# Kernel optimization log

Hardware: AMD Instinct MI355X
Metric: run time of the kernel (lower is better)

The kernel has to match this reference:

```python
import jax, jax.numpy as jnp
import numpy as np

N = 100000      # nodes
E = 1600000     # edges
G = 128         # graphs in batch
F_IN = 128
HID = 32
NCLS = 10


def _gcn_conv(x, src, dst, norm, W, b):
    # x: [N, Fin] -> [N, Fout]; src/dst/norm include self-loops: [E+N]
    h = x @ W                                   # dense transform first (Fout=32 < Fin)
    msg = h[src] * norm[:, None]                # gather + edge normalization
    out = jax.ops.segment_sum(msg, dst, num_segments=N)  # scatter-add
    return out + b


def setup_inputs() -> dict:
    key = jax.random.key(0)
    ks = jax.random.split(key, 10)
    x = jax.random.normal(ks[0], (N, F_IN), dtype=jnp.float32)
    edge_index = jax.random.randint(ks[1], (2, E), 0, N, dtype=jnp.int64)
    batch = jnp.sort(jax.random.randint(ks[2], (N,), 0, G, dtype=jnp.int64))
    s = 1.0 / np.sqrt(F_IN)
    W0 = jax.random.normal(ks[3], (F_IN, HID), dtype=jnp.float32) * s
    b0 = jnp.zeros((HID,), dtype=jnp.float32)
    sh = 1.0 / np.sqrt(HID)
    W1 = jax.random.normal(ks[4], (HID, HID), dtype=jnp.float32) * sh
    b1 = jnp.zeros((HID,), dtype=jnp.float32)
    W2 = jax.random.normal(ks[5], (HID, HID), dtype=jnp.float32) * sh
    b2 = jnp.zeros((HID,), dtype=jnp.float32)
    Wl = jax.random.normal(ks[6], (HID, NCLS), dtype=jnp.float32) * sh
    bl = jnp.zeros((NCLS,), dtype=jnp.float32)
    return {"x": x, "edge_index": edge_index, "batch": batch,
            "W0": W0, "b0": b0, "W1": W1, "b1": b1,
            "W2": W2, "b2": b2, "Wl": Wl, "bl": bl}


def reference(x, edge_index, batch, W0, b0, W1, b1, W2, b2, Wl, bl):
    # Self-loop augmented edge list (PyG GCNConv default: add_self_loops=True)
    loop = jnp.arange(N, dtype=edge_index.dtype)
    src = jnp.concatenate([edge_index[0], loop])    # [E+N]
    dst = jnp.concatenate([edge_index[1], loop])
    # Symmetric normalization D^{-1/2} (A+I) D^{-1/2}
    deg = jax.ops.segment_sum(jnp.ones_like(src, dtype=x.dtype), dst, num_segments=N)
    dinv = jax.lax.rsqrt(deg)                       # deg >= 1 thanks to self-loops
    norm = dinv[src] * dinv[dst]                    # [E+N]

    h = x
    for (W, b) in ((W0, b0), (W1, b1), (W2, b2)):
        h = jax.nn.relu(_gcn_conv(h, src, dst, norm, W, b))

    # global mean pool over graphs
    sums = jax.ops.segment_sum(h, batch, num_segments=G)           # [G, HID]
    cnts = jax.ops.segment_sum(jnp.ones((N,), h.dtype), batch, num_segments=G)
    pooled = sums / jnp.maximum(cnts, 1.0)[:, None]

    logits = jax.nn.relu(pooled @ Wl + bl)
    return jax.nn.log_softmax(logits, axis=1)
```

## Files before the change

### kernel.cpp

```cpp
#include <hip/hip_runtime.h>
#include <hip/hip_bf16.h>

#define NN 100000
#define NE 1600000
#define NG 128
#define FIN 128
#define HID 32
#define NCLS 10

#define EG4 (NE / 4)

#define NSL 32
#define GPS (EG4 / NSL)
#define RS 8
#define SUBN (NN / RS)
#define CSRGRID (RS * NSL)
#define CSR_T 1024

#define PAD 16
#define NEP (NE + NN * PAD + 64)

#define SCAN_B 1024
#define NB ((NN + SCAN_B - 1) / SCAN_B)

#define POOL_CHUNK 512
#define POOL_SEG 16
#define POOL_GSPAN 32
#define POOL_GRID ((NN + POOL_CHUNK - 1) / POOL_CHUNK)

#define G0_NODES 64
#define G0_GRID ((NN + G0_NODES - 1) / G0_NODES)
#define XPAD 136

#define AGG_GRID (NN / 4)
#define AGF_GRID (NN / 16)

typedef int int4v __attribute__((ext_vector_type(4)));
typedef __attribute__((ext_vector_type(8))) short short8;
typedef __attribute__((ext_vector_type(4))) float f32x4;

__device__ inline unsigned short f2bf(float f) {
    unsigned int u = __float_as_uint(f);
    unsigned int r = u + 0x7FFFu + ((u >> 16) & 1u);
    return (unsigned short)(r >> 16);
}
__device__ inline float bf2f(unsigned short v) {
    return __uint_as_float(((unsigned int)v) << 16);
}

__global__ void k_init(float* __restrict__ gsum, float* __restrict__ gcnt,
                       unsigned short* __restrict__ tzero,
                       unsigned short* __restrict__ hzero) {
    int i = blockIdx.x * blockDim.x + threadIdx.x;
    if (i < NG * HID) gsum[i] = 0.f;
    if (i < NG) gcnt[i] = 0.f;
    if (i < HID) { tzero[i] = 0; hzero[i] = 0; }
}

__global__ __launch_bounds__(CSR_T) void k_hist3(const int* __restrict__ dst,
                                                 unsigned char* __restrict__ partial) {
    const int r = blockIdx.x & (RS - 1);
    const int s = blockIdx.x >> 3;
    const int node0 = r * SUBN;
    __shared__ int lcnt[SUBN];
    for (int k = threadIdx.x; k < SUBN; k += CSR_T) lcnt[k] = 0;
    __syncthreads();
    const int g1 = (s + 1) * GPS;
    for (int g = s * GPS + threadIdx.x; g < g1; g += CSR_T) {
        const int4v d = *((const int4v*)dst + g);
        unsigned k;
        k = (unsigned)(d.x - node0); if (k < SUBN) atomicAdd(&lcnt[k], 1);
        k = (unsigned)(d.y - node0); if (k < SUBN) atomicAdd(&lcnt[k], 1);
        k = (unsigned)(d.z - node0); if (k < SUBN) atomicAdd(&lcnt[k], 1);
        k = (unsigned)(d.w - node0); if (k < SUBN) atomicAdd(&lcnt[k], 1);
    }
    __syncthreads();
    for (int k = threadIdx.x; k < SUBN; k += CSR_T)
        partial[s * NN + node0 + k] = (unsigned char)lcnt[k];
}

__global__ void k_scanA(unsigned char* __restrict__ partial, int* __restrict__ row_ptr,
                        int* __restrict__ bsum, float* __restrict__ dinv,
                        int* __restrict__ deg) {
    __shared__ int lds[SCAN_B];
    int i = blockIdx.x * SCAN_B + threadIdx.x;
    int pv = 0;
    if (i < NN) {
        int run = 0;
#pragma unroll
        for (int s = 0; s < NSL; s++) {
            int c = partial[s * NN + i];
            partial[s * NN + i] = (unsigned char)run;
            run += c;
        }
        deg[i] = run;
        dinv[i] = rsqrtf((float)run + 1.0f);
        pv = (run + PAD - 1) & ~(PAD - 1);
    }
    lds[threadIdx.x] = pv;
    __syncthreads();
    int val = pv;
    for (int off = 1; off < SCAN_B; off <<= 1) {
        int u = 0;
        if ((int)threadIdx.x >= off) u = lds[threadIdx.x - off];
        __syncthreads();
        if ((int)threadIdx.x >= off) { val += u; lds[threadIdx.x] = val; }
        __syncthreads();
    }
    if (i < NN) row_ptr[i] = val - pv;
    if (threadIdx.x == SCAN_B - 1) bsum[blockIdx.x] = val;
}

__global__ void k_scanB(int* __restrict__ bsum) {
    __shared__ int lds[128];
    int t = threadIdx.x;
    int v = (t < NB) ? bsum[t] : 0;
    lds[t] = v;
    __syncthreads();
    int val = v;
    for (int off = 1; off < 128; off <<= 1) {
        int u = 0;
        if (t >= off) u = lds[t - off];
        __syncthreads();
        if (t >= off) { val += u; lds[t] = val; }
        __syncthreads();
    }
    if (t < NB) bsum[t] = val - v;
}

__global__ void k_scanC(int* __restrict__ row_ptr, const int* __restrict__ bsum,
                        const int* __restrict__ deg, int* __restrict__ csr_src) {
    int i = blockIdx.x * SCAN_B + threadIdx.x;
    if (i < NN) {
        int r = row_ptr[i] + bsum[blockIdx.x];
        row_ptr[i] = r;
        int d = deg[i];
        int pd = (d + PAD - 1) & ~(PAD - 1);
        if (i == NN - 1) row_ptr[NN] = r + pd;
        for (int j = r + d; j < r + pd; j++) csr_src[j] = NN;
    }
}

__global__ __launch_bounds__(CSR_T) void k_scat3(const int* __restrict__ src,
                                                 const int* __restrict__ dst,
                                                 const int* __restrict__ row_ptr,
                                                 const unsigned char* __restrict__ pref,
                                                 int* __restrict__ csr_src) {
    const int r = blockIdx.x & (RS - 1);
    const int s = blockIdx.x >> 3;
    const int node0 = r * SUBN;
    __shared__ int lcur[SUBN];
    for (int k = threadIdx.x; k < SUBN; k += CSR_T)
        lcur[k] = row_ptr[node0 + k] + (int)pref[s * NN + node0 + k];
    __syncthreads();
    const int g1 = (s + 1) * GPS;
    for (int g = s * GPS + threadIdx.x; g < g1; g += CSR_T) {
        const int4v d = *((const int4v*)dst + g);
        const int4v sx = *((const int4v*)src + g);
        unsigned k;
        k = (unsigned)(d.x - node0); if (k < SUBN) { int p = atomicAdd(&lcur[k], 1); csr_src[p] = sx.x; }
        k = (unsigned)(d.y - node0); if (k < SUBN) { int p = atomicAdd(&lcur[k], 1); csr_src[p] = sx.y; }
        k = (unsigned)(d.z - node0); if (k < SUBN) { int p = atomicAdd(&lcur[k], 1); csr_src[p] = sx.z; }
        k = (unsigned)(d.w - node0); if (k < SUBN) { int p = atomicAdd(&lcur[k], 1); csr_src[p] = sx.w; }
    }
}

__global__ void k_gemm0(const float* __restrict__ x, const float* __restrict__ W,
                        const float* __restrict__ dinv, unsigned short* __restrict__ t) {
    __shared__ __align__(16) unsigned short x_lds[G0_NODES][XPAD];
    __shared__ __align__(16) unsigned short wt_lds[HID][XPAD];
    const int tid = threadIdx.x;
    const int node0 = blockIdx.x * G0_NODES;

#pragma unroll
    for (int r = 0; r < 8; r++) {
        int q = tid + 256 * r;
        int row = q >> 5;
        int c4 = q & 31;
        float4 xv = {0.f, 0.f, 0.f, 0.f};
        int node = node0 + row;
        if (node < NN) xv = ((const float4*)(x + (size_t)node * FIN))[c4];
        ushort4 b;
        b.x = f2bf(xv.x); b.y = f2bf(xv.y); b.z = f2bf(xv.z); b.w = f2bf(xv.w);
        *(ushort4*)&x_lds[row][c4 * 4] = b;
    }
#pragma unroll
    for (int r = 0; r < 16; r++) {
        int q = tid + 256 * r;
        int k = q >> 5, n = q & 31;
        wt_lds[n][k] = f2bf(W[q]);
    }
    __syncthreads();

    const int w = tid >> 6;
    const int lane = tid & 63;
    const int row = lane & 15;
    const int kg = lane >> 4;
    const int w16 = w * 16;

    f32x4 acc0 = {0.f, 0.f, 0.f, 0.f};
    f32x4 acc1 = {0.f, 0.f, 0.f, 0.f};
#pragma unroll
    for (int s = 0; s < 4; s++) {
        short8 a  = *(const short8*)&x_lds[w16 + row][s * 32 + kg * 8];
        short8 b0 = *(const short8*)&wt_lds[row][s * 32 + kg * 8];
        short8 b1 = *(const short8*)&wt_lds[16 + row][s * 32 + kg * 8];
        acc0 = __builtin_amdgcn_mfma_f32_16x16x32_bf16(a, b0, acc0, 0, 0, 0);
        acc1 = __builtin_amdgcn_mfma_f32_16x16x32_bf16(a, b1, acc1, 0, 0, 0);
    }

    const int f = lane & 15;
#pragma unroll
    for (int j = 0; j < 4; j++) {
        int node = node0 + w16 + kg * 4 + j;
        if (node < NN) {
            float di = dinv[node];
            t[(size_t)node * HID + f]      = f2bf(acc0[j] * di);
            t[(size_t)node * HID + 16 + f] = f2bf(acc1[j] * di);
        }
    }
}

__global__ __launch_bounds__(1024, 8) void k_aggf(const unsigned short* __restrict__ t,
                                                  const int* __restrict__ row_ptr,
                                                  const int* __restrict__ csr_src,
                                                  const float* __restrict__ dinv,
                                                  const float* __restrict__ b,
                                                  const float* __restrict__ Wn,
                                                  unsigned short* __restrict__ hout) {
    __shared__ __align__(16) unsigned short wt[HID][HID];
    __shared__ __align__(16) unsigned hlds[16 * 16];
    {
        int q = threadIdx.x;
        int k = q >> 5, n = q & 31;
        wt[n][k] = f2bf(Wn[q]);
    }
    const int wave = threadIdx.x >> 6;
    const int wid = blockIdx.x * 16 + wave;
    const int lane = threadIdx.x & 63;
    const int fp = lane & 15;
    const int sub = lane >> 4;
    const int beg = row_ptr[wid], end = row_ptr[wid + 1];
    const unsigned* twp = (const unsigned*)t;

    float accLo = 0.f, accHi = 0.f;
    if (sub == 0) {
        unsigned u = twp[(size_t)wid * 16 + fp];
        accLo = __uint_as_float(u << 16);
        accHi = __uint_as_float(u & 0xFFFF0000u);
    }
    int e = beg;
    int4v ia;
    if (e < end) ia = *(const int4v*)(csr_src + e + sub * 4);
    while (e < end) {
        const int4v ca = ia;
        const int en = e + 16;
        if (en < end) ia = *(const int4v*)(csr_src + en + sub * 4);
        unsigned u0 = twp[(size_t)ca.x * 16 + fp];
        unsigned u1 = twp[(size_t)ca.y * 16 + fp];
        unsigned u2 = twp[(size_t)ca.z * 16 + fp];
        unsigned u3 = twp[(size_t)ca.w * 16 + fp];
        accLo += __uint_as_float(u0 << 16);
        accHi += __uint_as_float(u0 & 0xFFFF0000u);
        accLo += __uint_as_float(u1 << 16);
        accHi += __uint_as_float(u1 & 0xFFFF0000u);
        accLo += __uint_as_float(u2 << 16);
        accHi += __uint_as_float(u2 & 0xFFFF0000u);
        accLo += __uint_as_float(u3 << 16);
        accHi += __uint_as_float(u3 & 0xFFFF0000u);
        e = en;
    }
    accLo += __shfl_xor(accLo, 16, 64);
    accHi += __shfl_xor(accHi, 16, 64);
    accLo += __shfl_xor(accLo, 32, 64);
    accHi += __shfl_xor(accHi, 32, 64);

    if (lane < 16) {
        const float di = dinv[wid];
        float hLo = fmaxf(fmaf(accLo, di, b[2 * fp]), 0.f);
        float hHi = fmaxf(fmaf(accHi, di, b[2 * fp + 1]), 0.f);
        hlds[wave * 16 + fp] = (unsigned)f2bf(hLo) | ((unsigned)f2bf(hHi) << 16);
    }
    __syncthreads();
    if (threadIdx.x >= 64) return;

    const int row = lane & 15;
    const int kg = lane >> 4;
    short8 a  = *(const short8*)((const unsigned short*)hlds + row * 32 + kg * 8);
    short8 b0 = *(const short8*)&wt[row][kg * 8];
    short8 b1 = *(const short8*)&wt[16 + row][kg * 8];
    f32x4 d0 = {0.f, 0.f, 0.f, 0.f};
    f32x4 d1 = {0.f, 0.f, 0.f, 0.f};
    d0 = __builtin_amdgcn_mfma_f32_16x16x32_bf16(a, b0, d0, 0, 0, 0);
    d1 = __builtin_amdgcn_mfma_f32_16x16x32_bf16(a, b1, d1, 0, 0, 0);
    const int node0 = blockIdx.x * 16;
#pragma unroll
    for (int j = 0; j < 4; j++) {
        int node = node0 + kg * 4 + j;
        float dv = dinv[node];
        hout[(size_t)node * HID + row]      = f2bf(d0[j] * dv);
        hout[(size_t)node * HID + 16 + row] = f2bf(d1[j] * dv);
    }
}

__global__ __launch_bounds__(256, 8) void k_agga(const unsigned short* __restrict__ t,
                                                 const int* __restrict__ row_ptr,
                                                 const int* __restrict__ csr_src,
                                                 const float* __restrict__ dinv,
                                                 const float* __restrict__ b,
                                                 unsigned short* __restrict__ hout) {
    const int wid = (blockIdx.x * 256 + threadIdx.x) >> 6;
    if (wid >= NN) return;
    const int lane = threadIdx.x & 63;
    const int fp = lane & 15;
    const int sub = lane >> 4;
    const int beg = row_ptr[wid], end = row_ptr[wid + 1];
    const unsigned* tw = (const unsigned*)t;

    float accLo = 0.f, accHi = 0.f;
    if (sub == 0) {
        unsigned u = tw[(size_t)wid * 16 + fp];
        accLo = __uint_as_float(u << 16);
        accHi = __uint_as_float(u & 0xFFFF0000u);
    }
    int e = beg;
    int4v ia;
    if (e < end) ia = *(const int4v*)(csr_src + e + sub * 4);
    while (e < end) {
        const int4v ca = ia;
        const int en = e + 16;
        if (en < end) ia = *(const int4v*)(csr_src + en + sub * 4);
        unsigned u0 = tw[(size_t)ca.x * 16 + fp];
        unsigned u1 = tw[(size_t)ca.y * 16 + fp];
        unsigned u2 = tw[(size_t)ca.z * 16 + fp];
        unsigned u3 = tw[(size_t)ca.w * 16 + fp];
        accLo += __uint_as_float(u0 << 16);
        accHi += __uint_as_float(u0 & 0xFFFF0000u);
        accLo += __uint_as_float(u1 << 16);
        accHi += __uint_as_float(u1 & 0xFFFF0000u);
        accLo += __uint_as_float(u2 << 16);
        accHi += __uint_as_float(u2 & 0xFFFF0000u);
        accLo += __uint_as_float(u3 << 16);
        accHi += __uint_as_float(u3 & 0xFFFF0000u);
        e = en;
    }
    accLo += __shfl_xor(accLo, 16, 64);
    accHi += __shfl_xor(accHi, 16, 64);
    accLo += __shfl_xor(accLo, 32, 64);
    accHi += __shfl_xor(accHi, 32, 64);
    if (sub == 0) {
        float di = dinv[wid];
        float rLo = fmaxf(fmaf(accLo, di, b[2 * fp]), 0.f);
        float rHi = fmaxf(fmaf(accHi, di, b[2 * fp + 1]), 0.f);
        unsigned out = (unsigned)f2bf(rLo) | ((unsigned)f2bf(rHi) << 16);
        ((unsigned*)hout)[(size_t)wid * 16 + fp] = out;
    }
}

__global__ void k_pool2(const unsigned short* __restrict__ h, const int* __restrict__ batch,
                        float* __restrict__ gsum, float* __restrict__ gcnt) {
    __shared__ float lacc[POOL_GSPAN][HID];
    __shared__ float lcnt[POOL_GSPAN];
    __shared__ int s_gmin;
    const int chunk_start = blockIdx.x * POOL_CHUNK;

    for (int j = threadIdx.x; j < POOL_GSPAN * HID; j += 256) ((float*)lacc)[j] = 0.f;
    if (threadIdx.x < POOL_GSPAN) lcnt[threadIdx.x] = 0.f;
    if (threadIdx.x == 0) {
        int cs = chunk_start < NN ? chunk_start : NN - 1;
        s_gmin = batch[cs];
    }
    __syncthreads();
    const int gmin = s_gmin;

    const int seg = threadIdx.x >> 3;
    const int l = (threadIdx.x & 7) * 4;
    const int i0 = chunk_start + seg * POOL_SEG;

    float4 acc = {0.f, 0.f, 0.f, 0.f};
    float cnt = 0.f;
    int cur_g = -1;

    for (int k = 0; k < POOL_SEG; k++) {
        int i = i0 + k;
        if (i >= NN) break;
        int g = batch[i];
        if (g != cur_g) {
            if (cur_g >= 0) {
                int bin = cur_g - gmin;
                if (bin >= 0 && bin < POOL_GSPAN) {
                    atomicAdd(&lacc[bin][l + 0], acc.x);
                    atomicAdd(&lacc[bin][l + 1], acc.y);
                    atomicAdd(&lacc[bin][l + 2], acc.z);
                    atomicAdd(&lacc[bin][l + 3], acc.w);
                    if (l == 0) atomicAdd(&lcnt[bin], cnt);
                } else {
                    atomicAdd(&gsum[cur_g * HID + l + 0], acc.x);
                    atomicAdd(&gsum[cur_g * HID + l + 1], acc.y);
                    atomicAdd(&gsum[cur_g * HID + l + 2], acc.z);
                    atomicAdd(&gsum[cur_g * HID + l + 3], acc.w);
                    if (l == 0) atomicAdd(&gcnt[cur_g], cnt);
                }
            }
            cur_g = g;
            acc.x = acc.y = acc.z = acc.w = 0.f;
            cnt = 0.f;
        }
        const ushort4 v = *(const ushort4*)&h[(size_t)i * HID + l];
        acc.x += bf2f(v.x); acc.y += bf2f(v.y);
        acc.z += bf2f(v.z); acc.w += bf2f(v.w);
        cnt += 1.f;
    }
    if (cur_g >= 0) {
        int bin = cur_g - gmin;
        if (bin >= 0 && bin < POOL_GSPAN) {
            atomicAdd(&lacc[bin][l + 0], acc.x);
            atomicAdd(&lacc[bin][l + 1], acc.y);
            atomicAdd(&lacc[bin][l + 2], acc.z);
            atomicAdd(&lacc[bin][l + 3], acc.w);
            if (l == 0) atomicAdd(&lcnt[bin], cnt);
        } else {
            atomicAdd(&gsum[cur_g * HID + l + 0], acc.x);
            atomicAdd(&gsum[cur_g * HID + l + 1], acc.y);
            atomicAdd(&gsum[cur_g * HID + l + 2], acc.z);
            atomicAdd(&gsum[cur_g * HID + l + 3], acc.w);
            if (l == 0) atomicAdd(&gcnt[cur_g], cnt);
        }
    }
    __syncthreads();

    for (int j = threadIdx.x; j < POOL_GSPAN * HID; j += 256) {
        int bin = j / HID, f = j % HID;
        int g = gmin + bin;
        float v = lacc[bin][f];
        if (g < NG && v != 0.f) atomicAdd(&gsum[g * HID + f], v);
    }
    if (threadIdx.x < POOL_GSPAN) {
        int g = gmin + threadIdx.x;
        float c = lcnt[threadIdx.x];
        if (g < NG && c != 0.f) atomicAdd(&gcnt[g], c);
    }
}

__global__ void k_classify(const float* __restrict__ gsum, const float* __restrict__ gcnt,
                           const float* __restrict__ Wl, const float* __restrict__ bl,
                           float* __restrict__ out) {
    __shared__ float w[HID * NCLS];
    __shared__ float bb[NCLS];
    int t = threadIdx.x;
    for (int j = t; j < HID * NCLS; j += blockDim.x) w[j] = Wl[j];
    if (t < NCLS) bb[t] = bl[t];
    __syncthreads();
    if (t >= NG) return;
    float c = gcnt[t];
    c = c > 1.f ? c : 1.f;
    float p[HID];
#pragma unroll
    for (int k = 0; k < HID; k++) p[k] = gsum[t * HID + k] / c;
    float lg[NCLS];
    float m = -1e30f;
#pragma unroll
    for (int c2 = 0; c2 < NCLS; c2++) {
        float a = bb[c2];
#pragma unroll
        for (int k = 0; k < HID; k++) a = fmaf(p[k], w[k * NCLS + c2], a);
        a = a > 0.f ? a : 0.f;
        lg[c2] = a;
        m = fmaxf(m, a);
    }
    float s = 0.f;
#pragma unroll
    for (int c2 = 0; c2 < NCLS; c2++) s += expf(lg[c2] - m);
    float ls = logf(s);
#pragma unroll
    for (int c2 = 0; c2 < NCLS; c2++) out[t * NCLS + c2] = lg[c2] - m - ls;
}

extern "C" void kernel_launch(void* const* d_in, const int* in_sizes, int n_in,
                              void* d_out, int out_size, void* d_ws, size_t ws_size,
                              hipStream_t stream) {
    const float* x  = (const float*)d_in[0];
    const int* ei   = (const int*)d_in[1];
    const int* batch = (const int*)d_in[2];
    const float* W0 = (const float*)d_in[3];
    const float* b0 = (const float*)d_in[4];
    const float* W1 = (const float*)d_in[5];
    const float* b1 = (const float*)d_in[6];
    const float* W2 = (const float*)d_in[7];
    const float* b2 = (const float*)d_in[8];
    const float* Wl = (const float*)d_in[9];
    const float* bl = (const float*)d_in[10];
    float* out = (float*)d_out;

    const int* esrc = ei;
    const int* edst = ei + NE;

    char* ws = (char*)d_ws;
    size_t off = 0;
    auto alloc = [&](size_t bytes) -> void* {
        void* p = ws + off;
        off = (off + bytes + 511) & ~(size_t)511;
        return p;
    };
    int*   row_ptr = (int*)alloc((NN + 1) * sizeof(int));
    float* dinv    = (float*)alloc(NN * sizeof(float));
    int*   deg     = (int*)alloc(NN * sizeof(int));
    int*   bsum    = (int*)alloc(256 * sizeof(int));
    int*   csr_src = (int*)alloc((size_t)NEP * sizeof(int));
    unsigned short* tbuf = (unsigned short*)alloc((size_t)(NN + 1) * HID * sizeof(unsigned short));
    unsigned short* hA   = (unsigned short*)alloc((size_t)(NN + 1) * HID * sizeof(unsigned short));
    float* gsum    = (float*)alloc(NG * HID * sizeof(float));
    float* gcnt    = (float*)alloc(NG * sizeof(float));
    (void)ws_size; (void)in_sizes; (void)n_in; (void)out_size;

    unsigned char* partial = (unsigned char*)tbuf;
    unsigned short* tzero = tbuf + (size_t)NN * HID;
    unsigned short* hzero = hA + (size_t)NN * HID;

    k_init<<<17, 256, 0, stream>>>(gsum, gcnt, tzero, hzero);
    k_hist3<<<CSRGRID, CSR_T, 0, stream>>>(edst, partial);
    k_scanA<<<NB, SCAN_B, 0, stream>>>(partial, row_ptr, bsum, dinv, deg);
    k_scanB<<<1, 128, 0, stream>>>(bsum);
    k_scanC<<<NB, SCAN_B, 0, stream>>>(row_ptr, bsum, deg, csr_src);
    k_scat3<<<CSRGRID, CSR_T, 0, stream>>>(esrc, edst, row_ptr, partial, csr_src);

    k_gemm0<<<G0_GRID, 256, 0, stream>>>(x, W0, dinv, tbuf);
    k_aggf<<<AGF_GRID, 1024, 0, stream>>>(tbuf, row_ptr, csr_src, dinv, b0, W1, hA);
    k_aggf<<<AGF_GRID, 1024, 0, stream>>>(hA, row_ptr, csr_src, dinv, b1, W2, tbuf);
    k_agga<<<AGG_GRID, 256, 0, stream>>>(tbuf, row_ptr, csr_src, dinv, b2, hA);

    k_pool2<<<POOL_GRID, 256, 0, stream>>>(hA, batch, gsum, gcnt);
    k_classify<<<1, 128, 0, stream>>>(gsum, gcnt, Wl, bl, out);
}
```

Baseline: 198.3 us.

## Software-pipeline neighbor gathers and halve aggregation block size

The gather loop in both aggregation kernels now uses a two-stage software pipeline. It loads feature rows for the next 16-edge window and indices for the one after while accumulating the current window, so more memory requests are in flight per wave. The fused aggregate-plus-GEMM kernel now uses 512-thread blocks that handle 8 nodes each. It zero-pads the unused half of the LDS tile for the MFMA and skips stores for the unused rows. The cost is higher register pressure from the extra prefetch registers, plus the weight-transpose setup repeated across twice as many blocks.

```diff
diff --git a/kernel.cpp b/kernel.cpp
--- a/kernel.cpp
+++ b/kernel.cpp
@@ -33,7 +33,8 @@
 #define XPAD 136
 
 #define AGG_GRID (NN / 4)
-#define AGF_GRID (NN / 16)
+#define AGF_NPB 8
+#define AGF_GRID (NN / AGF_NPB)
 
 typedef int int4v __attribute__((ext_vector_type(4)));
 typedef __attribute__((ext_vector_type(8))) short short8;
@@ -221,22 +222,23 @@
     }
 }
 
-__global__ __launch_bounds__(1024, 8) void k_aggf(const unsigned short* __restrict__ t,
-                                                  const int* __restrict__ row_ptr,
-                                                  const int* __restrict__ csr_src,
-                                                  const float* __restrict__ dinv,
-                                                  const float* __restrict__ b,
-                                                  const float* __restrict__ Wn,
-                                                  unsigned short* __restrict__ hout) {
+__global__ __launch_bounds__(512, 8) void k_aggf(const unsigned short* __restrict__ t,
+                                                 const int* __restrict__ row_ptr,
+                                                 const int* __restrict__ csr_src,
+                                                 const float* __restrict__ dinv,
+                                                 const float* __restrict__ b,
+                                                 const float* __restrict__ Wn,
+                                                 unsigned short* __restrict__ hout) {
     __shared__ __align__(16) unsigned short wt[HID][HID];
     __shared__ __align__(16) unsigned hlds[16 * 16];
-    {
-        int q = threadIdx.x;
-        int k = q >> 5, n = q & 31;
-        wt[n][k] = f2bf(Wn[q]);
-    }
+    for (int q = threadIdx.x; q < HID * HID; q += 512) {
+        int n = q >> 5, k = q & 31;
+        wt[n][k] = f2bf(Wn[k * HID + n]);
+    }
+    if (threadIdx.x < 128) hlds[128 + threadIdx.x] = 0;
+
     const int wave = threadIdx.x >> 6;
-    const int wid = blockIdx.x * 16 + wave;
+    const int wid = blockIdx.x * AGF_NPB + wave;
     const int lane = threadIdx.x & 63;
     const int fp = lane & 15;
     const int sub = lane >> 4;
@@ -249,26 +251,40 @@
         accLo = __uint_as_float(u << 16);
         accHi = __uint_as_float(u & 0xFFFF0000u);
     }
-    int e = beg;
-    int4v ia;
-    if (e < end) ia = *(const int4v*)(csr_src + e + sub * 4);
-    while (e < end) {
-        const int4v ca = ia;
-        const int en = e + 16;
-        if (en < end) ia = *(const int4v*)(csr_src + en + sub * 4);
-        unsigned u0 = twp[(size_t)ca.x * 16 + fp];
-        unsigned u1 = twp[(size_t)ca.y * 16 + fp];
-        unsigned u2 = twp[(size_t)ca.z * 16 + fp];
-        unsigned u3 = twp[(size_t)ca.w * 16 + fp];
-        accLo += __uint_as_float(u0 << 16);
-        accHi += __uint_as_float(u0 & 0xFFFF0000u);
-        accLo += __uint_as_float(u1 << 16);
-        accHi += __uint_as_float(u1 & 0xFFFF0000u);
-        accLo += __uint_as_float(u2 << 16);
-        accHi += __uint_as_float(u2 & 0xFFFF0000u);
-        accLo += __uint_as_float(u3 << 16);
-        accHi += __uint_as_float(u3 & 0xFFFF0000u);
-        e = en;
+
+    const int nwin = (end - beg) >> 4;
+    int e = beg + sub * 4;
+    int4v iaC = {0, 0, 0, 0}, iaN = {0, 0, 0, 0};
+    if (nwin > 0) iaC = *(const int4v*)(csr_src + e);
+    if (nwin > 1) iaN = *(const int4v*)(csr_src + e + 16);
+    unsigned c0 = 0, c1 = 0, c2 = 0, c3 = 0;
+    if (nwin > 0) {
+        c0 = twp[(size_t)iaC.x * 16 + fp];
+        c1 = twp[(size_t)iaC.y * 16 + fp];
+        c2 = twp[(size_t)iaC.z * 16 + fp];
+        c3 = twp[(size_t)iaC.w * 16 + fp];
+    }
+    for (int w = 0; w < nwin; w++) {
+        unsigned n0 = 0, n1 = 0, n2 = 0, n3 = 0;
+        if (w + 1 < nwin) {
+            n0 = twp[(size_t)iaN.x * 16 + fp];
+            n1 = twp[(size_t)iaN.y * 16 + fp];
+            n2 = twp[(size_t)iaN.z * 16 + fp];
+            n3 = twp[(size_t)iaN.w * 16 + fp];
+        }
+        int4v iaP = iaN;
+        if (w + 2 < nwin) iaP = *(const int4v*)(csr_src + e + 32);
+        accLo += __uint_as_float(c0 << 16);
+        accHi += __uint_as_float(c0 & 0xFFFF0000u);
+        accLo += __uint_as_float(c1 << 16);
+        accHi += __uint_as_float(c1 & 0xFFFF0000u);
+        accLo += __uint_as_float(c2 << 16);
+        accHi += __uint_as_float(c2 & 0xFFFF0000u);
+        accLo += __uint_as_float(c3 << 16);
+        accHi += __uint_as_float(c3 & 0xFFFF0000u);
+        c0 = n0; c1 = n1; c2 = n2; c3 = n3;
+        iaN = iaP;
+        e += 16;
     }
     accLo += __shfl_xor(accLo, 16, 64);
     accHi += __shfl_xor(accHi, 16, 64);
@@ -293,7 +309,8 @@
     f32x4 d1 = {0.f, 0.f, 0.f, 0.f};
     d0 = __builtin_amdgcn_mfma_f32_16x16x32_bf16(a, b0, d0, 0, 0, 0);
     d1 = __builtin_amdgcn_mfma_f32_16x16x32_bf16(a, b1, d1, 0, 0, 0);
-    const int node0 = blockIdx.x * 16;
+    if (kg >= 2) return;
+    const int node0 = blockIdx.x * AGF_NPB;
 #pragma unroll
     for (int j = 0; j < 4; j++) {
         int node = node0 + kg * 4 + j;
@@ -323,26 +340,40 @@
         accLo = __uint_as_float(u << 16);
         accHi = __uint_as_float(u & 0xFFFF0000u);
     }
-    int e = beg;
-    int4v ia;
-    if (e < end) ia = *(const int4v*)(csr_src + e + sub * 4);
-    while (e < end) {
-        const int4v ca = ia;
-        const int en = e + 16;
-        if (en < end) ia = *(const int4v*)(csr_src + en + sub * 4);
-        unsigned u0 = tw[(size_t)ca.x * 16 + fp];
-        unsigned u1 = tw[(size_t)ca.y * 16 + fp];
-        unsigned u2 = tw[(size_t)ca.z * 16 + fp];
-        unsigned u3 = tw[(size_t)ca.w * 16 + fp];
-        accLo += __uint_as_float(u0 << 16);
-        accHi += __uint_as_float(u0 & 0xFFFF0000u);
-        accLo += __uint_as_float(u1 << 16);
-        accHi += __uint_as_float(u1 & 0xFFFF0000u);
-        accLo += __uint_as_float(u2 << 16);
-        accHi += __uint_as_float(u2 & 0xFFFF0000u);
-        accLo += __uint_as_float(u3 << 16);
-        accHi += __uint_as_float(u3 & 0xFFFF0000u);
-        e = en;
+
+    const int nwin = (end - beg) >> 4;
+    int e = beg + sub * 4;
+    int4v iaC = {0, 0, 0, 0}, iaN = {0, 0, 0, 0};
+    if (nwin > 0) iaC = *(const int4v*)(csr_src + e);
+    if (nwin > 1) iaN = *(const int4v*)(csr_src + e + 16);
+    unsigned c0 = 0, c1 = 0, c2 = 0, c3 = 0;
+    if (nwin > 0) {
+        c0 = tw[(size_t)iaC.x * 16 + fp];
+        c1 = tw[(size_t)iaC.y * 16 + fp];
+        c2 = tw[(size_t)iaC.z * 16 + fp];
+        c3 = tw[(size_t)iaC.w * 16 + fp];
+    }
+    for (int w = 0; w < nwin; w++) {
+        unsigned n0 = 0, n1 = 0, n2 = 0, n3 = 0;
+        if (w + 1 < nwin) {
+            n0 = tw[(size_t)iaN.x * 16 + fp];
+            n1 = tw[(size_t)iaN.y * 16 + fp];
+            n2 = tw[(size_t)iaN.z * 16 + fp];
+            n3 = tw[(size_t)iaN.w * 16 + fp];
+        }
+        int4v iaP = iaN;
+        if (w + 2 < nwin) iaP = *(const int4v*)(csr_src + e + 32);
+        accLo += __uint_as_float(c0 << 16);
+        accHi += __uint_as_float(c0 & 0xFFFF0000u);
+        accLo += __uint_as_float(c1 << 16);
+        accHi += __uint_as_float(c1 & 0xFFFF0000u);
+        accLo += __uint_as_float(c2 << 16);
+        accHi += __uint_as_float(c2 & 0xFFFF0000u);
+        accLo += __uint_as_float(c3 << 16);
+        accHi += __uint_as_float(c3 & 0xFFFF0000u);
+        c0 = n0; c1 = n1; c2 = n2; c3 = n3;
+        iaN = iaP;
+        e += 16;
     }
     accLo += __shfl_xor(accLo, 16, 64);
     accHi += __shfl_xor(accHi, 16, 64);
@@ -525,8 +556,8 @@
     k_scat3<<<CSRGRID, CSR_T, 0, stream>>>(esrc, edst, row_ptr, partial, csr_src);
 
     k_gemm0<<<G0_GRID, 256, 0, stream>>>(x, W0, dinv, tbuf);
-    k_aggf<<<AGF_GRID, 1024, 0, stream>>>(tbuf, row_ptr, csr_src, dinv, b0, W1, hA);
-    k_aggf<<<AGF_GRID, 1024, 0, stream>>>(hA, row_ptr, csr_src, dinv, b1, W2, tbuf);
+    k_aggf<<<AGF_GRID, 512, 0, stream>>>(tbuf, row_ptr, csr_src, dinv, b0, W1, hA);
+    k_aggf<<<AGF_GRID, 512, 0, stream>>>(hA, row_ptr, csr_src, dinv, b1, W2, tbuf);
     k_agga<<<AGG_GRID, 256, 0, stream>>>(tbuf, row_ptr, csr_src, dinv, b2, hA);
 
     k_pool2<<<POOL_GRID, 256, 0, stream>>>(hA, batch, gsum, gcnt);
```

Result: slower. 213.0 us (+7.4%).
